# Optimization experiments

Hardware: AMD Instinct MI355X
Metric: run time of the kernel (lower is better)

The kernel has to match this reference:

```python
import jax, jax.numpy as jnp
import numpy as np

KERNEL = 3
PAD = 1
GRID_SIZE = 5
SPLINE_ORDER = 3
GRID_LO, GRID_HI = -1.0, 1.0
IN_CH, OUT_CH = 8, 16
IN_FEATURES = IN_CH * KERNEL ** 3  # 216


def make_grid(in_features, dtype=jnp.float32):
    # buffer from KANLinear.__init__: uniform knots extended by spline_order on each side
    h = (GRID_HI - GRID_LO) / GRID_SIZE
    g = jnp.arange(-SPLINE_ORDER, GRID_SIZE + SPLINE_ORDER + 1, dtype=dtype) * h + GRID_LO
    return jnp.broadcast_to(g, (in_features, g.shape[0]))  # (in, G+2k+1)


def b_splines(x, grid):
    # x: (M, in) -> bases: (M, in, G+k) via Cox-de Boor recursion
    x = x[..., None]  # (M, in, 1)
    bases = ((x >= grid[:, :-1]) & (x < grid[:, 1:])).astype(x.dtype)
    for k in range(1, SPLINE_ORDER + 1):
        left = (x - grid[:, : -(k + 1)]) / (grid[:, k:-1] - grid[:, : -(k + 1)])
        right = (grid[:, k + 1:] - x) / (grid[:, k + 1:] - grid[:, 1:-k])
        bases = left * bases[..., :-1] + right * bases[..., 1:]
    return bases


def unfold3d(x, k, pad):
    # torch unfoldNd ordering: feature dim = (C, kd, kh, kw) flattened, channel slowest
    N, C, D, H, W = x.shape
    xp = jnp.pad(x, ((0, 0), (0, 0), (pad, pad), (pad, pad), (pad, pad)))
    Do, Ho, Wo = D + 2 * pad - k + 1, H + 2 * pad - k + 1, W + 2 * pad - k + 1
    patches = []
    for i in range(k):
        for j in range(k):
            for l in range(k):
                patches.append(xp[:, :, i:i + Do, j:j + Ho, l:l + Wo])
    p = jnp.stack(patches, axis=2)  # (N, C, k^3, Do, Ho, Wo)
    return p.reshape(N, C * k ** 3, Do * Ho * Wo), (Do, Ho, Wo)


def reference(x, base_weight, spline_weight, spline_scaler):
    N = x.shape[0]
    blocks, (Do, Ho, Wo) = unfold3d(x, KERNEL, PAD)     # (N, F, L)
    blocks = blocks.transpose(0, 2, 1).reshape(-1, IN_FEATURES)  # (N*L, F)

    grid = make_grid(IN_FEATURES, blocks.dtype)
    base_out = jnp.matmul(jax.nn.silu(blocks), base_weight.T)       # (M, out)
    scaled_w = spline_weight * spline_scaler[..., None]             # (out, in, G+k)
    bases = b_splines(blocks, grid)                                 # (M, in, G+k)
    spline_out = jnp.einsum('mic,oic->mo', bases, scaled_w)
    out = base_out + spline_out                                     # (M, out)

    out = out.reshape(N, -1, OUT_CH).transpose(0, 2, 1)             # (N, out, L)
    return out.reshape(N, OUT_CH, Do, Ho, Wo)


def setup_inputs() -> dict:
    key = jax.random.key(0)
    k1, k2, k3, k4 = jax.random.split(key, 4)
    x = jax.random.normal(k1, (1, IN_CH, 32, 32, 32), dtype=jnp.float32)
    base_weight = jax.random.normal(k2, (OUT_CH, IN_FEATURES), dtype=jnp.float32) * 0.05
    spline_weight = jax.random.normal(k3, (OUT_CH, IN_FEATURES, GRID_SIZE + SPLINE_ORDER), dtype=jnp.float32) * 0.05
    spline_scaler = jax.random.normal(k4, (OUT_CH, IN_FEATURES), dtype=jnp.float32) * 0.05 + 1.0
    return {"x": x, "base_weight": base_weight, "spline_weight": spline_weight, "spline_scaler": spline_scaler}
```

## Files before the change

kernel.cpp:

```cpp
#include <hip/hip_runtime.h>
#include <math.h>

#define IN_CH   8
#define OUT_CH  16
#define DIM     32
#define PDIM    34
#define NBASES  8
#define NF      216
#define LTOT    32768
#define TPAD    12
#define KVOX    96

typedef _Float16 half8 __attribute__((ext_vector_type(8)));
typedef float    f32x4 __attribute__((ext_vector_type(4)));

__device__ __forceinline__ float knot(int j) {
    return (float)(j - 3) * 0.4f + (-1.0f);
}

__device__ __forceinline__ void eval_bases(float v, float b[11]) {
    #pragma unroll
    for (int j = 0; j < 11; ++j)
        b[j] = (v >= knot(j) && v < knot(j + 1)) ? 1.0f : 0.0f;
    #pragma unroll
    for (int k = 1; k <= 3; ++k) {
        #pragma unroll
        for (int j = 0; j + k < 11; ++j) {
            float rl = 1.0f / (knot(j + k)     - knot(j));
            float rr = 1.0f / (knot(j + k + 1) - knot(j + 1));
            b[j] = (v - knot(j)) * rl * b[j]
                 + (knot(j + k + 1) - v) * rr * b[j + 1];
        }
    }
}

__device__ __forceinline__ float silu(float v) {
    return v / (1.0f + __expf(-v));
}

__global__ void prep_weights(const float* __restrict__ bw,
                             const float* __restrict__ sw,
                             const float* __restrict__ sc,
                             _Float16* __restrict__ Wt) {
    int id = blockIdx.x * blockDim.x + threadIdx.x;
    if (id >= 27 * 3 * 16 * 32) return;
    int kl  = id & 31;
    int o   = (id >> 5) & 15;
    int tq  = id >> 9;
    int q   = tq % 3;
    int tap = tq / 3;
    int k = q * 32 + kl;
    int cch = k / TPAD, t = k % TPAD;
    float val = 0.0f;
    if (t < 9) {
        int wi = o * NF + (cch * 27 + tap);
        val = (t == 0) ? bw[wi] : sw[(size_t)wi * NBASES + (t - 1)] * sc[wi];
    }
    Wt[id] = (_Float16)val;
}

__global__ __launch_bounds__(256) void conv_fused(const float* __restrict__ x,
                                                  const _Float16* __restrict__ Wt,
                                                  float* __restrict__ out) {
    __shared__ __align__(16) _Float16 lf[288 * KVOX];
    int bx = blockIdx.x;
    int x0 = (bx & 1) * 16;
    int y0 = ((bx >> 1) & 15) * 2;
    int z0 = (bx >> 5) * 2;
    int tid = threadIdx.x;

    #pragma unroll
    for (int it = 0; it < 9; ++it) {
        int i = tid + it * 256;
        int c = i / 288;
        int v = i % 288;
        int lx = v % 18;
        int t2 = v / 18;
        int ly = t2 & 3, lz = t2 >> 2;
        int xp = x0 + lx, yp = y0 + ly, zp = z0 + lz;
        float val = 0.0f;
        if (xp >= 1 && xp <= DIM && yp >= 1 && yp <= DIM && zp >= 1 && zp <= DIM)
            val = x[((c * DIM + (zp - 1)) * DIM + (yp - 1)) * DIM + (xp - 1)];
        float b[11];
        eval_bases(val, b);
        __align__(8) _Float16 h[TPAD];
        h[0] = (_Float16)silu(val);
        #pragma unroll
        for (int j = 0; j < NBASES; ++j) h[1 + j] = (_Float16)b[j];
        h[9] = (_Float16)0.f; h[10] = (_Float16)0.f; h[11] = (_Float16)0.f;
        uint2* d = (uint2*)(lf + (size_t)v * KVOX + c * TPAD);
        d[0] = *(uint2*)&h[0];
        d[1] = *(uint2*)&h[4];
        d[2] = *(uint2*)&h[8];
    }
    __syncthreads();

    int lane = tid & 63;
    int w    = tid >> 6;
    int yw = w & 1, zw = w >> 1;
    int po = lane & 15;
    int kq = lane >> 4;
    f32x4 acc = {0.f, 0.f, 0.f, 0.f};

    #pragma unroll
    for (int kd = 0; kd < 3; ++kd) {
        #pragma unroll
        for (int kh = 0; kh < 3; ++kh) {
            const _Float16* lrow = lf + ((zw + kd) * 4 + (yw + kh)) * (18 * KVOX);
            #pragma unroll
            for (int kw = 0; kw < 3; ++kw) {
                #pragma unroll
                for (int q = 0; q < 3; ++q) {
                    int tap = (kd * 3 + kh) * 3 + kw;
                    half8 a = *(const half8*)(Wt + ((tap * 3 + q) * 16 + po) * 32 + kq * 8);
                    half8 b = *(const half8*)(lrow + (po + kw) * KVOX + q * 32 + kq * 8);
                    acc = __builtin_amdgcn_mfma_f32_16x16x32_f16(a, b, acc, 0, 0, 0);
                }
            }
        }
    }

    int pos = ((z0 + zw) * 32 + (y0 + yw)) * 32 + x0 + po;
    #pragma unroll
    for (int r = 0; r < 4; ++r)
        out[(size_t)(kq * 4 + r) * LTOT + pos] = acc[r];
}

__global__ __launch_bounds__(64) void fused_kernel(const float* __restrict__ x,
                                                   const float* __restrict__ bw,
                                                   const float* __restrict__ sw,
                                                   const float* __restrict__ sc,
                                                   float* __restrict__ out) {
    int p = blockIdx.x * 64 + threadIdx.x;
    int xo = p & 31;
    int yo = (p >> 5) & 31;
    int zo = p >> 10;
    float acc[OUT_CH];
    #pragma unroll
    for (int o = 0; o < OUT_CH; ++o) acc[o] = 0.0f;
    for (int c = 0; c < IN_CH; ++c)
        for (int kd = 0; kd < 3; ++kd)
            for (int kh = 0; kh < 3; ++kh)
                for (int kw = 0; kw < 3; ++kw) {
                    int zi = zo + kd - 1, yi = yo + kh - 1, xi = xo + kw - 1;
                    float v = 0.0f;
                    if (zi >= 0 && zi < DIM && yi >= 0 && yi < DIM && xi >= 0 && xi < DIM)
                        v = x[((c * DIM + zi) * DIM + yi) * DIM + xi];
                    float b[11];
                    eval_bases(v, b);
                    float s = silu(v);
                    int i = c * 27 + kd * 9 + kh * 3 + kw;
                    #pragma unroll
                    for (int o = 0; o < OUT_CH; ++o) {
                        int wi = o * NF + i;
                        float dot = 0.0f;
                        #pragma unroll
                        for (int j = 0; j < NBASES; ++j)
                            dot += b[j] * sw[(size_t)wi * NBASES + j];
                        acc[o] += s * bw[wi] + sc[wi] * dot;
                    }
                }
    #pragma unroll
    for (int o = 0; o < OUT_CH; ++o)
        out[(size_t)o * LTOT + p] = acc[o];
}

extern "C" void kernel_launch(void* const* d_in, const int* in_sizes, int n_in,
                              void* d_out, int out_size, void* d_ws, size_t ws_size,
                              hipStream_t stream) {
    const float* x  = (const float*)d_in[0];
    const float* bw = (const float*)d_in[1];
    const float* sw = (const float*)d_in[2];
    const float* sc = (const float*)d_in[3];
    float* out = (float*)d_out;

    const size_t W_bytes = (size_t)27 * 3 * 16 * 32 * 2;
    if (ws_size >= W_bytes) {
        _Float16* Wt = (_Float16*)d_ws;
        prep_weights<<<(27 * 3 * 16 * 32 + 255) / 256, 256, 0, stream>>>(bw, sw, sc, Wt);
        conv_fused<<<512, 256, 0, stream>>>(x, Wt, out);
    } else {
        fused_kernel<<<512, 64, 0, stream>>>(x, bw, sw, sc, out);
    }
}
```

Measured before the change: 78.41 us.

## Replace Cox-de Boor recursion with closed-form uniform cubic B-spline and batch channel loads

Per-voxel basis evaluation now computes only the four nonzero uniform cubic B-spline weights in closed form and scatters them into the zeroed record, instead of running the full 11-entry Cox-de Boor recursion. The staging loop is restructured so each thread loads all 8 channels of one voxel up front, then handles one extra (channel, voxel) pair from the tail. SiLU uses a hardware reciprocal. This removes most of the staging ALU work. The cost is extra scattered 16-bit LDS stores and possible small numerical differences at knot boundaries.

```diff
diff --git a/kernel.cpp b/kernel.cpp
--- a/kernel.cpp
+++ b/kernel.cpp
@@ -32,10 +32,6 @@
                  + (knot(j + k + 1) - v) * rr * b[j + 1];
         }
     }
-}
-
-__device__ __forceinline__ float silu(float v) {
-    return v / (1.0f + __expf(-v));
 }
 
 __global__ void prep_weights(const float* __restrict__ bw,
@@ -59,6 +55,37 @@
     Wt[id] = (_Float16)val;
 }
 
+__device__ __forceinline__ void stage_one(_Float16* __restrict__ rec, float val) {
+    float s = val * __builtin_amdgcn_rcpf(1.0f + __expf(-val));
+    union { _Float16 h[4]; uint2 q; } w0;
+    w0.h[0] = (_Float16)s; w0.h[1] = (_Float16)0.f;
+    w0.h[2] = (_Float16)0.f; w0.h[3] = (_Float16)0.f;
+    uint2* r64 = (uint2*)rec;
+    r64[0] = w0.q;
+    r64[1] = make_uint2(0u, 0u);
+    r64[2] = make_uint2(0u, 0u);
+    float cf = (val + 2.2f) * 2.5f;
+    cf = fminf(fmaxf(cf, -1.0f), 12.0f);
+    float fj = floorf(cf);
+    int   cj = (int)fj;
+    float u  = cf - fj;
+    float um = 1.0f - u;
+    float u2 = u * u, u3 = u2 * u;
+    float q0 = u3 * (1.0f / 6.0f);
+    float q1 = (1.0f + 3.0f * u + 3.0f * u2 - 3.0f * u3) * (1.0f / 6.0f);
+    float q2 = (4.0f - 6.0f * u2 + 3.0f * u3) * (1.0f / 6.0f);
+    float q3 = um * um * um * (1.0f / 6.0f);
+    int j0 = cj - 3;
+    int t0 = ((unsigned)(j0    ) <= 7u) ? (j0 + 1) : 9;
+    int t1 = ((unsigned)(j0 + 1) <= 7u) ? (j0 + 2) : 9;
+    int t2 = ((unsigned)(j0 + 2) <= 7u) ? (j0 + 3) : 9;
+    int t3 = ((unsigned)(j0 + 3) <= 7u) ? (j0 + 4) : 9;
+    rec[t0] = (_Float16)q3;
+    rec[t1] = (_Float16)q2;
+    rec[t2] = (_Float16)q1;
+    rec[t3] = (_Float16)q0;
+}
+
 __global__ __launch_bounds__(256) void conv_fused(const float* __restrict__ x,
                                                   const _Float16* __restrict__ Wt,
                                                   float* __restrict__ out) {
@@ -69,29 +96,31 @@
     int z0 = (bx >> 5) * 2;
     int tid = threadIdx.x;
 
-    #pragma unroll
-    for (int it = 0; it < 9; ++it) {
-        int i = tid + it * 256;
-        int c = i / 288;
-        int v = i % 288;
-        int lx = v % 18;
-        int t2 = v / 18;
-        int ly = t2 & 3, lz = t2 >> 2;
+    {
+        int v   = tid;
+        int lx  = v % 18;
+        int row = v / 18;
+        int ly = row & 3, lz = row >> 2;
         int xp = x0 + lx, yp = y0 + ly, zp = z0 + lz;
-        float val = 0.0f;
-        if (xp >= 1 && xp <= DIM && yp >= 1 && yp <= DIM && zp >= 1 && zp <= DIM)
-            val = x[((c * DIM + (zp - 1)) * DIM + (yp - 1)) * DIM + (xp - 1)];
-        float b[11];
-        eval_bases(val, b);
-        __align__(8) _Float16 h[TPAD];
-        h[0] = (_Float16)silu(val);
-        #pragma unroll
-        for (int j = 0; j < NBASES; ++j) h[1 + j] = (_Float16)b[j];
-        h[9] = (_Float16)0.f; h[10] = (_Float16)0.f; h[11] = (_Float16)0.f;
-        uint2* d = (uint2*)(lf + (size_t)v * KVOX + c * TPAD);
-        d[0] = *(uint2*)&h[0];
-        d[1] = *(uint2*)&h[4];
-        d[2] = *(uint2*)&h[8];
+        bool inr = (xp >= 1 && xp <= DIM && yp >= 1 && yp <= DIM && zp >= 1 && zp <= DIM);
+        int gbase = (((zp - 1) * DIM + (yp - 1)) * DIM) + (xp - 1);
+        float vals[IN_CH];
+        #pragma unroll
+        for (int c = 0; c < IN_CH; ++c)
+            vals[c] = inr ? x[gbase + c * (DIM * DIM * DIM)] : 0.0f;
+        #pragma unroll
+        for (int c = 0; c < IN_CH; ++c)
+            stage_one(lf + (size_t)v * KVOX + c * TPAD, vals[c]);
+
+        int c2  = tid >> 5;
+        int v2  = 256 + (tid & 31);
+        int lx2 = v2 % 18;
+        int row2 = v2 / 18;
+        int ly2 = row2 & 3, lz2 = row2 >> 2;
+        int xp2 = x0 + lx2, yp2 = y0 + ly2, zp2 = z0 + lz2;
+        bool inr2 = (xp2 >= 1 && xp2 <= DIM && yp2 >= 1 && yp2 <= DIM && zp2 >= 1 && zp2 <= DIM);
+        float v2val = inr2 ? x[(((c2 * DIM + (zp2 - 1)) * DIM + (yp2 - 1)) * DIM) + (xp2 - 1)] : 0.0f;
+        stage_one(lf + (size_t)v2 * KVOX + c2 * TPAD, v2val);
     }
     __syncthreads();
 
@@ -148,7 +177,7 @@
                         v = x[((c * DIM + zi) * DIM + yi) * DIM + xi];
                     float b[11];
                     eval_bases(v, b);
-                    float s = silu(v);
+                    float s = v * __builtin_amdgcn_rcpf(1.0f + __expf(-v));
                     int i = c * 27 + kd * 9 + kh * 3 + kw;
                     #pragma unroll
                     for (int o = 0; o < OUT_CH; ++o) {
```

After: 77.65 us. No clear change (-1.0%).
